# Kernel tuning notes

Hardware: AMD Instinct MI355X
Metric: run time of the kernel (lower is better)

## Reference

```python
import jax, jax.numpy as jnp
import numpy as np

B, S, D, H = 4, 4096, 1024, 16
LOCAL_W, GLOBAL_W = 128, 1024


def _mha_window(x, w_in, b_in, w_out, b_out, window, n_heads):
    # Faithful port of sliding_window_attention + nn.MultiheadAttention self-attn.
    b, s, d = x.shape
    nw = (s + window - 1) // window
    pad = nw * window - s
    xp = jnp.pad(x, ((0, 0), (0, pad), (0, 0))) if pad > 0 else x
    xw = xp.reshape(b * nw, window, d)                      # [b*nw, w, d]
    qkv = xw @ w_in.T + b_in                                # [b*nw, w, 3d]
    q, k, v = jnp.split(qkv, 3, axis=-1)
    dh = d // n_heads
    q = q.reshape(-1, window, n_heads, dh)
    k = k.reshape(-1, window, n_heads, dh)
    v = v.reshape(-1, window, n_heads, dh)
    # NOTE: torch code passes a FLOAT triu(ones) mask -> it is ADDED to logits
    # (adds +1.0 above the diagonal), not -inf causal masking. Replicated exactly.
    add_mask = jnp.triu(jnp.ones((window, window), dtype=x.dtype), k=1)
    scores = jnp.einsum('bqhd,bkhd->bhqk', q, k) / np.sqrt(dh).astype(x.dtype)
    scores = scores + add_mask
    attn = jax.nn.softmax(scores, axis=-1)
    o = jnp.einsum('bhqk,bkhd->bqhd', attn, v).reshape(-1, window, d)
    o = o @ w_out.T + b_out
    return o.reshape(b, nw * window, d)[:, :s, :]


def setup_inputs() -> dict:
    key = jax.random.key(0)
    ks = jax.random.split(key, 10)
    sc = 0.02
    inp = {
        'lqs': jax.random.normal(ks[0], (B, S, D), jnp.float32),
        'gqs': jax.random.normal(ks[1], (B, S, D), jnp.float32),
        'wl_in': jax.random.normal(ks[2], (3 * D, D), jnp.float32) * sc,
        'bl_in': jnp.zeros((3 * D,), jnp.float32),
        'wl_out': jax.random.normal(ks[3], (D, D), jnp.float32) * sc,
        'bl_out': jnp.zeros((D,), jnp.float32),
        'wg_in': jax.random.normal(ks[4], (3 * D, D), jnp.float32) * sc,
        'bg_in': jnp.zeros((3 * D,), jnp.float32),
        'wg_out': jax.random.normal(ks[5], (D, D), jnp.float32) * sc,
        'bg_out': jnp.zeros((D,), jnp.float32),
    }
    return inp


def reference(lqs, gqs, wl_in, bl_in, wl_out, bl_out, wg_in, bg_in, wg_out, bg_out):
    local_out = _mha_window(lqs, wl_in, bl_in, wl_out, bl_out, LOCAL_W, H)
    global_out = _mha_window(gqs, wg_in, bg_in, wg_out, bg_out, GLOBAL_W, H)
    return (local_out, global_out)
```

## Files before the change

### kernel.cpp

```cpp
#include <hip/hip_runtime.h>
#include <stdint.h>

typedef short v8s __attribute__((ext_vector_type(8)));
typedef float v4f __attribute__((ext_vector_type(4)));

__device__ __forceinline__ unsigned short f2bf(float f) {
    union { float f; uint32_t u; } x; x.f = f;
    uint32_t r = (x.u + 0x7fffu + ((x.u >> 16) & 1u)) >> 16;
    return (unsigned short)r;
}
__device__ __forceinline__ uint32_t pack_bf2(float lo, float hi) {
    union { float f; uint32_t u; } a, b; a.f = lo; b.f = hi;
    uint32_t rl = (a.u + 0x7fffu + ((a.u >> 16) & 1u)) >> 16;
    uint32_t rh = (b.u + 0x7fffu + ((b.u >> 16) & 1u)) & 0xffff0000u;
    return rh | rl;
}

__global__ __launch_bounds__(256) void cast_f32_bf16(const float* __restrict__ in,
                                                     unsigned short* __restrict__ out, int n) {
    int i = (blockIdx.x * 256 + threadIdx.x) * 4;
    const int stride = gridDim.x * 256 * 4;
    for (; i < n; i += stride) {
        float4 v = *(const float4*)(in + i);
        ushort4 o;
        o.x = f2bf(v.x); o.y = f2bf(v.y); o.z = f2bf(v.z); o.w = f2bf(v.w);
        *(ushort4*)(out + i) = o;
    }
}

template <bool OUT_F32, bool VSPLIT>
__global__ __launch_bounds__(256) void gemm_nt(const unsigned short* __restrict__ A,
                                               const unsigned short* __restrict__ B,
                                               const float* __restrict__ bias,
                                               void* __restrict__ Cout,
                                               unsigned short* __restrict__ vt,
                                               int M, int N, int K, int ldc) {
    __shared__ unsigned short As[128 * 64];
    __shared__ unsigned short Bs[128 * 64];
    const int tid = threadIdx.x;
    const int wv = tid >> 6, lane = tid & 63;
    const int quad = lane >> 4, l16 = lane & 15;
    const int tiles_n = N >> 7;
    const int tm = blockIdx.x / tiles_n, tn = blockIdx.x - tm * tiles_n;
    const int m0 = tm << 7, n0 = tn << 7;
    const int wr = (wv >> 1) * 64, wc = (wv & 1) * 64;

    v4f acc[4][4] = {};

    for (int k0 = 0; k0 < K; k0 += 64) {
        __syncthreads();
#pragma unroll
        for (int j = 0; j < 4; ++j) {
            const int cb = (wv * 4 + j) * 64;
            const int cl = cb + lane;
            const int row = cl >> 3;
            const int kc = (cl & 7) ^ (row & 7);
            const unsigned short* ga = A + (size_t)(m0 + row) * K + k0 + kc * 8;
            const unsigned short* gb = B + (size_t)(n0 + row) * K + k0 + kc * 8;
            __builtin_amdgcn_global_load_lds(
                (const __attribute__((address_space(1))) unsigned int*)ga,
                (__attribute__((address_space(3))) unsigned int*)(As + cb * 8), 16, 0, 0);
            __builtin_amdgcn_global_load_lds(
                (const __attribute__((address_space(1))) unsigned int*)gb,
                (__attribute__((address_space(3))) unsigned int*)(Bs + cb * 8), 16, 0, 0);
        }
        __syncthreads();
#pragma unroll
        for (int ks = 0; ks < 2; ++ks) {
            v8s af[4], bf[4];
#pragma unroll
            for (int mt = 0; mt < 4; ++mt) {
                const int row = wr + mt * 16 + l16;
                const int ch = row * 8 + ((ks * 4 + quad) ^ (row & 7));
                af[mt] = *(const v8s*)(As + ch * 8);
            }
#pragma unroll
            for (int nt = 0; nt < 4; ++nt) {
                const int row = wc + nt * 16 + l16;
                const int ch = row * 8 + ((ks * 4 + quad) ^ (row & 7));
                bf[nt] = *(const v8s*)(Bs + ch * 8);
            }
#pragma unroll
            for (int mt = 0; mt < 4; ++mt)
#pragma unroll
                for (int nt = 0; nt < 4; ++nt)
                    acc[mt][nt] = __builtin_amdgcn_mfma_f32_16x16x32_bf16(
                        af[mt], bf[nt], acc[mt][nt], 0, 0, 0);
        }
    }
#pragma unroll
    for (int nt = 0; nt < 4; ++nt) {
        const int col = n0 + wc + nt * 16 + l16;
        const float bv = bias[col];
        if (VSPLIT && col >= 2048) {
#pragma unroll
            for (int mt = 0; mt < 4; ++mt) {
                const int rowb = m0 + wr + mt * 16 + quad * 4;
                ushort4 o;
                o.x = f2bf(acc[mt][nt][0] + bv);
                o.y = f2bf(acc[mt][nt][1] + bv);
                o.z = f2bf(acc[mt][nt][2] + bv);
                o.w = f2bf(acc[mt][nt][3] + bv);
                *(ushort4*)(vt + (size_t)(col - 2048) * M + rowb) = o;
            }
        } else {
#pragma unroll
            for (int mt = 0; mt < 4; ++mt) {
                const int rowb = m0 + wr + mt * 16 + quad * 4;
#pragma unroll
                for (int r = 0; r < 4; ++r) {
                    if (OUT_F32)
                        ((float*)Cout)[(size_t)(rowb + r) * ldc + col] = acc[mt][nt][r] + bv;
                    else
                        ((unsigned short*)Cout)[(size_t)(rowb + r) * ldc + col] =
                            f2bf(acc[mt][nt][r] + bv);
                }
            }
        }
    }
}

__global__ __launch_bounds__(256, 3) void attn_win(const unsigned short* __restrict__ qk,
                                                   const unsigned short* __restrict__ Vt,
                                                   unsigned short* __restrict__ O,
                                                   int W) {
    const int nkt = W >> 7;
    const int tid = threadIdx.x, wv = tid >> 6, lane = tid & 63;
    const int quad = lane >> 4, l16 = lane & 15;

    int wh, qb;
    if (nkt == 8) {
        const int g = blockIdx.x;
        wh = (g >> 6) * 8 + (g & 7);
        qb = (g >> 3) & 7;
    } else {
        wh = blockIdx.x; qb = 0;
    }
    const int winst = wh >> 4, head = wh & 15;
    const size_t rw = (size_t)winst * W;

    __shared__ unsigned short Ks[128 * 64];
    __shared__ unsigned short Vs[64 * 128];
    __shared__ unsigned short Ps[4 * 16 * 136];
    unsigned short* Pw = Ps + wv * 16 * 136;

    v8s qf[2][2];
#pragma unroll
    for (int st = 0; st < 2; ++st) {
        const size_t qrow = rw + (size_t)(qb * 128 + wv * 32 + st * 16 + l16);
        const unsigned short* qp = qk + qrow * 2048 + head * 64 + quad * 8;
        qf[st][0] = *(const v8s*)qp;
        qf[st][1] = *(const v8s*)(qp + 32);
    }

    float rsum[2] = {0.f, 0.f};
    v4f oacc[2][4] = {};

    for (int kt = 0; kt < nkt; ++kt) {
        __syncthreads();
#pragma unroll
        for (int j = 0; j < 4; ++j) {
            const int cb = (wv * 4 + j) * 64;
            const int cl = cb + lane;
            const int key = cl >> 3, c = cl & 7;
            const unsigned short* src = qk + (rw + (size_t)(kt * 128 + key)) * 2048
                                        + 1024 + head * 64 + ((c ^ (key & 7)) * 8);
            __builtin_amdgcn_global_load_lds(
                (const __attribute__((address_space(1))) unsigned int*)src,
                (__attribute__((address_space(3))) unsigned int*)(Ks + cb * 8), 16, 0, 0);
        }
#pragma unroll
        for (int j = 0; j < 4; ++j) {
            const int cb = (wv * 4 + j) * 64;
            const int cl = cb + lane;
            const int dh = cl >> 4, c = cl & 15;
            const unsigned short* src = Vt + (size_t)(head * 64 + dh) * 16384
                                        + rw + (size_t)(kt * 128) + ((c ^ (dh & 7)) * 8);
            __builtin_amdgcn_global_load_lds(
                (const __attribute__((address_space(1))) unsigned int*)src,
                (__attribute__((address_space(3))) unsigned int*)(Vs + cb * 8), 16, 0, 0);
        }
        __syncthreads();

        v4f sf[2][8] = {};
#pragma unroll
        for (int nt = 0; nt < 8; ++nt) {
            const int krow = nt * 16 + l16;
#pragma unroll
            for (int ks = 0; ks < 2; ++ks) {
                const v8s kf = *(const v8s*)(Ks + krow * 64 + ((ks * 4 + quad) ^ (krow & 7)) * 8);
                sf[0][nt] = __builtin_amdgcn_mfma_f32_16x16x32_bf16(kf, qf[0][ks], sf[0][nt], 0, 0, 0);
                sf[1][nt] = __builtin_amdgcn_mfma_f32_16x16x32_bf16(kf, qf[1][ks], sf[1][nt], 0, 0, 0);
            }
        }

#pragma unroll
        for (int st = 0; st < 2; ++st) {
            const int irow = qb * 128 + wv * 32 + st * 16 + l16;
            float rl = 0.f;
#pragma unroll
            for (int nt = 0; nt < 8; ++nt) {
                const int jb = kt * 128 + nt * 16 + quad * 4;
                float e[4];
#pragma unroll
                for (int r = 0; r < 4; ++r)
                    e[r] = __expf(fmaf(sf[st][nt][r], 0.125f, (jb + r > irow) ? 1.0f : 0.0f));
                rl += (e[0] + e[1]) + (e[2] + e[3]);
                uint2 pk;
                pk.x = pack_bf2(e[0], e[1]);
                pk.y = pack_bf2(e[2], e[3]);
                *(uint2*)(Pw + l16 * 136 + nt * 16 + quad * 4) = pk;
            }
            rsum[st] += rl;
#pragma unroll
            for (int kk = 0; kk < 4; ++kk) {
                const v8s pf = *(const v8s*)(Pw + l16 * 136 + kk * 32 + quad * 8);
#pragma unroll
                for (int dt = 0; dt < 4; ++dt) {
                    const int dh = dt * 16 + l16;
                    const v8s vf = *(const v8s*)(Vs + dh * 128 + ((kk * 4 + quad) ^ (dh & 7)) * 8);
                    oacc[st][dt] = __builtin_amdgcn_mfma_f32_16x16x32_bf16(pf, vf, oacc[st][dt], 0, 0, 0);
                }
            }
        }
    }

#pragma unroll
    for (int st = 0; st < 2; ++st) {
        float l = rsum[st];
        l += __shfl_xor(l, 16);
        l += __shfl_xor(l, 32);
        const float inv = 1.0f / l;
#pragma unroll
        for (int r = 0; r < 4; ++r) {
            const float invr = __shfl(inv, quad * 4 + r);
            const size_t row = rw + (size_t)(qb * 128 + wv * 32 + st * 16 + quad * 4 + r);
#pragma unroll
            for (int dt = 0; dt < 4; ++dt)
                O[row * 1024 + head * 64 + dt * 16 + l16] = f2bf(oacc[st][dt][r] * invr);
        }
    }
}

extern "C" void kernel_launch(void* const* d_in, const int* in_sizes, int n_in,
                              void* d_out, int out_size, void* d_ws, size_t ws_size,
                              hipStream_t stream) {
    const float* lqs    = (const float*)d_in[0];
    const float* gqs    = (const float*)d_in[1];
    const float* wl_in  = (const float*)d_in[2];
    const float* bl_in  = (const float*)d_in[3];
    const float* wl_out = (const float*)d_in[4];
    const float* bl_out = (const float*)d_in[5];
    const float* wg_in  = (const float*)d_in[6];
    const float* bg_in  = (const float*)d_in[7];
    const float* wg_out = (const float*)d_in[8];
    const float* bg_out = (const float*)d_in[9];

    char* ws = (char*)d_ws;
    unsigned short* Xbf    = (unsigned short*)(ws);
    unsigned short* Obf    = (unsigned short*)(ws + 33554432);
    unsigned short* Winbf  = (unsigned short*)(ws + 67108864);
    unsigned short* Woutbf = (unsigned short*)(ws + 73400320);
    unsigned short* QKbf   = (unsigned short*)(ws + 75497472);
    unsigned short* Vtbf   = (unsigned short*)(ws + 142606336);

    const int R = 4 * 4096;
    const int D = 1024;

    for (int path = 0; path < 2; ++path) {
        const float* x     = path == 0 ? lqs : gqs;
        const float* w_in  = path == 0 ? wl_in : wg_in;
        const float* b_in  = path == 0 ? bl_in : bg_in;
        const float* w_out = path == 0 ? wl_out : wg_out;
        const float* b_out = path == 0 ? bl_out : bg_out;
        const int W        = path == 0 ? 128 : 1024;
        float* outp = (float*)d_out + (size_t)path * R * D;

        hipLaunchKernelGGL(cast_f32_bf16, dim3(4096), dim3(256), 0, stream, x, Xbf, R * D);
        hipLaunchKernelGGL(cast_f32_bf16, dim3(3072), dim3(256), 0, stream, w_in, Winbf, 3 * D * D);
        hipLaunchKernelGGL(cast_f32_bf16, dim3(1024), dim3(256), 0, stream, w_out, Woutbf, D * D);
        hipLaunchKernelGGL((gemm_nt<false, true>), dim3(128 * 24), dim3(256), 0, stream,
                           Xbf, Winbf, b_in, (void*)QKbf, Vtbf, R, 3 * D, D, 2048);
        hipLaunchKernelGGL(attn_win, dim3(2048), dim3(256), 0, stream, QKbf, Vtbf, Obf, W);
        hipLaunchKernelGGL((gemm_nt<true, false>), dim3(128 * 8), dim3(256), 0, stream,
                           Obf, Woutbf, b_out, (void*)outp, (unsigned short*)nullptr,
                           R, D, D, 1024);
    }
}
```

Measured before the change: 786.2 us.

## Fold softmax scale and log2e into Q projection and use exp2 with packed bf16 convert

```diff
diff --git a/kernel.cpp b/kernel.cpp
--- a/kernel.cpp
+++ b/kernel.cpp
@@ -9,12 +9,14 @@
     uint32_t r = (x.u + 0x7fffu + ((x.u >> 16) & 1u)) >> 16;
     return (unsigned short)r;
 }
-__device__ __forceinline__ uint32_t pack_bf2(float lo, float hi) {
-    union { float f; uint32_t u; } a, b; a.f = lo; b.f = hi;
-    uint32_t rl = (a.u + 0x7fffu + ((a.u >> 16) & 1u)) >> 16;
-    uint32_t rh = (b.u + 0x7fffu + ((b.u >> 16) & 1u)) & 0xffff0000u;
-    return rh | rl;
-}
+__device__ __forceinline__ uint32_t cvt_pk_bf16(float lo, float hi) {
+    uint32_t r;
+    asm("v_cvt_pk_bf16_f32 %0, %1, %2" : "=v"(r) : "v"(lo), "v"(hi));
+    return r;
+}
+
+#define QSCALE 0.18033688011112042f
+#define L2E    1.4426950408889634f
 
 __global__ __launch_bounds__(256) void cast_f32_bf16(const float* __restrict__ in,
                                                      unsigned short* __restrict__ out, int n) {
@@ -104,6 +106,7 @@
                 *(ushort4*)(vt + (size_t)(col - 2048) * M + rowb) = o;
             }
         } else {
+            const float scl = (VSPLIT && col < 1024) ? QSCALE : 1.0f;
 #pragma unroll
             for (int mt = 0; mt < 4; ++mt) {
                 const int rowb = m0 + wr + mt * 16 + quad * 4;
@@ -113,7 +116,7 @@
                         ((float*)Cout)[(size_t)(rowb + r) * ldc + col] = acc[mt][nt][r] + bv;
                     else
                         ((unsigned short*)Cout)[(size_t)(rowb + r) * ldc + col] =
-                            f2bf(acc[mt][nt][r] + bv);
+                            f2bf((acc[mt][nt][r] + bv) * scl);
                 }
             }
         }
@@ -127,6 +130,7 @@
     const int nkt = W >> 7;
     const int tid = threadIdx.x, wv = tid >> 6, lane = tid & 63;
     const int quad = lane >> 4, l16 = lane & 15;
+    const int wvu = __builtin_amdgcn_readfirstlane(wv);
 
     int wh, qb;
     if (nkt == 8) {
@@ -143,6 +147,10 @@
     __shared__ unsigned short Vs[64 * 128];
     __shared__ unsigned short Ps[4 * 16 * 136];
     unsigned short* Pw = Ps + wv * 16 * 136;
+
+    float bmix[4];
+#pragma unroll
+    for (int r = 0; r < 4; ++r) bmix[r] = (quad * 4 + r > l16) ? L2E : 0.0f;
 
     v8s qf[2][2];
 #pragma unroll
@@ -196,19 +204,28 @@
 
 #pragma unroll
         for (int st = 0; st < 2; ++st) {
-            const int irow = qb * 128 + wv * 32 + st * 16 + l16;
+            const int qbase = qb * 128 + wvu * 32 + st * 16;
             float rl = 0.f;
 #pragma unroll
             for (int nt = 0; nt < 8; ++nt) {
-                const int jb = kt * 128 + nt * 16 + quad * 4;
-                float e[4];
-#pragma unroll
-                for (int r = 0; r < 4; ++r)
-                    e[r] = __expf(fmaf(sf[st][nt][r], 0.125f, (jb + r > irow) ? 1.0f : 0.0f));
-                rl += (e[0] + e[1]) + (e[2] + e[3]);
+                const int jb0 = kt * 128 + nt * 16;
+                float e0, e1, e2, e3;
+                if (jb0 == qbase) {
+                    e0 = exp2f(sf[st][nt][0] + bmix[0]);
+                    e1 = exp2f(sf[st][nt][1] + bmix[1]);
+                    e2 = exp2f(sf[st][nt][2] + bmix[2]);
+                    e3 = exp2f(sf[st][nt][3] + bmix[3]);
+                } else {
+                    const float b = (jb0 > qbase) ? L2E : 0.0f;
+                    e0 = exp2f(sf[st][nt][0] + b);
+                    e1 = exp2f(sf[st][nt][1] + b);
+                    e2 = exp2f(sf[st][nt][2] + b);
+                    e3 = exp2f(sf[st][nt][3] + b);
+                }
+                rl += (e0 + e1) + (e2 + e3);
                 uint2 pk;
-                pk.x = pack_bf2(e[0], e[1]);
-                pk.y = pack_bf2(e[2], e[3]);
+                pk.x = cvt_pk_bf16(e0, e1);
+                pk.y = cvt_pk_bf16(e2, e3);
                 *(uint2*)(Pw + l16 * 136 + nt * 16 + quad * 4) = pk;
             }
             rsum[st] += rl;
```

Measured after the change: 961.3 us. 22.3% more time.
